# Optimization experiments

Hardware: AMD Instinct MI355X
Metric: run time of the kernel (lower is better)

Reference implementation:

```python
import jax, jax.numpy as jnp
import numpy as np

N_NODES = 50000
NEG_SLOPE = 0.2  # PyG GATConv default leaky-relu slope


def _gat_conv(x, edge_index, W, a_src, a_dst, bias, heads, out_ch, concat, num_nodes):
    # x: [N, F_in]; W: [F_in, heads*out_ch]; a_src/a_dst: [heads, out_ch]; bias: [heads*out_ch] or [out_ch]
    h = (x @ W).reshape(num_nodes, heads, out_ch)            # [N,H,C]
    alpha_src = jnp.einsum('nhc,hc->nh', h, a_src)           # [N,H]
    alpha_dst = jnp.einsum('nhc,hc->nh', h, a_dst)           # [N,H]
    src, dst = edge_index[0], edge_index[1]
    e = jax.nn.leaky_relu(alpha_src[src] + alpha_dst[dst], NEG_SLOPE)  # [E,H]
    # segment softmax over incoming edges per destination (self-loops guarantee non-empty segments)
    m = jax.ops.segment_max(e, dst, num_segments=num_nodes)
    e = jnp.exp(e - m[dst])
    denom = jax.ops.segment_sum(e, dst, num_segments=num_nodes)
    alpha = e / denom[dst]                                    # [E,H]
    msg = h[src] * alpha[:, :, None]                          # [E,H,C]
    out = jax.ops.segment_sum(msg, dst, num_segments=num_nodes)  # [N,H,C]
    if concat:
        out = out.reshape(num_nodes, heads * out_ch)
    else:
        out = out.mean(axis=1)
    return out + bias


def _add_self_loops(edge_index, num_nodes):
    loops = jnp.arange(num_nodes, dtype=edge_index.dtype)
    return jnp.concatenate([edge_index, jnp.stack([loops, loops])], axis=1)


def setup_inputs() -> dict:
    key = jax.random.key(0)
    ks = jax.random.split(key, 16)
    N, F_in, H, C_hid, C_out = N_NODES, 128, 4, 64, 64
    E = 800000
    x = jax.random.normal(ks[0], (N, F_in), dtype=jnp.float32)
    edge_index = jax.random.randint(ks[1], (2, E), 0, N, dtype=jnp.int32)
    s = lambda fan: 1.0 / np.sqrt(fan)
    inp = {
        'x': x, 'edge_index': edge_index,
        'W1': jax.random.normal(ks[2], (F_in, H * C_hid), jnp.float32) * s(F_in),
        'a_src1': jax.random.normal(ks[3], (H, C_hid), jnp.float32) * s(C_hid),
        'a_dst1': jax.random.normal(ks[4], (H, C_hid), jnp.float32) * s(C_hid),
        'b1': jnp.zeros((H * C_hid,), jnp.float32),
        'W2': jax.random.normal(ks[5], (H * C_hid, H * C_hid), jnp.float32) * s(H * C_hid),
        'a_src2': jax.random.normal(ks[6], (H, C_hid), jnp.float32) * s(C_hid),
        'a_dst2': jax.random.normal(ks[7], (H, C_hid), jnp.float32) * s(C_hid),
        'b2': jnp.zeros((H * C_hid,), jnp.float32),
        'W3': jax.random.normal(ks[8], (H * C_hid, C_out), jnp.float32) * s(H * C_hid),
        'a_src3': jax.random.normal(ks[9], (1, C_out), jnp.float32) * s(C_out),
        'a_dst3': jax.random.normal(ks[10], (1, C_out), jnp.float32) * s(C_out),
        'b3': jnp.zeros((C_out,), jnp.float32),
    }
    return inp


def reference(x, edge_index, W1, a_src1, a_dst1, b1, W2, a_src2, a_dst2, b2, W3, a_src3, a_dst3, b3):
    N = x.shape[0]
    ei = _add_self_loops(edge_index, N)
    h = _gat_conv(x, ei, W1, a_src1, a_dst1, b1, heads=4, out_ch=64, concat=True, num_nodes=N)
    h = jax.nn.elu(h)
    h = _gat_conv(h, ei, W2, a_src2, a_dst2, b2, heads=4, out_ch=64, concat=True, num_nodes=N)
    h = jax.nn.elu(h)
    out = _gat_conv(h, ei, W3, a_src3, a_dst3, b3, heads=1, out_ch=64, concat=False, num_nodes=N)
    return out
```

## Files before the change

### kernel.cpp

```cpp
#include <hip/hip_runtime.h>
#include <hip/hip_fp16.h>
#include <cstdint>


typedef _Float16 f16;
typedef _Float16 f16x8 __attribute__((ext_vector_type(8)));
typedef float f32x4 __attribute__((ext_vector_type(4)));

__global__ __launch_bounds__(256) void count_kernel(const int* __restrict__ ei,
                                                    int E, int N,
                                                    int* __restrict__ deg) {
  int g = blockIdx.x * 256 + threadIdx.x;
  if (g >= E + N) return;
  int dst = (g < E) ? ei[E + g] : (g - E);
  atomicAdd(&deg[dst], 1);
}

__global__ __launch_bounds__(256) void deg_block_reduce(const int* __restrict__ deg,
                                                        int* __restrict__ bsum, int N) {
  __shared__ int red[4];
  int b = blockIdx.x;
  int v = 0;
#pragma unroll
  for (int s = 0; s < 4; ++s) {
    int idx = b * 1024 + s * 256 + threadIdx.x;
    if (idx < N) v += deg[idx];
  }
  for (int off = 32; off; off >>= 1) v += __shfl_down(v, off);
  if ((threadIdx.x & 63) == 0) red[threadIdx.x >> 6] = v;
  __syncthreads();
  if (threadIdx.x == 0) bsum[b] = red[0] + red[1] + red[2] + red[3];
}

__global__ __launch_bounds__(1024) void small_scan(const int* __restrict__ bsum,
                                                   int* __restrict__ bpre, int NB) {
  __shared__ int buf[1024];
  int v = (threadIdx.x < NB) ? bsum[threadIdx.x] : 0;
  buf[threadIdx.x] = v;
  __syncthreads();
  for (int off = 1; off < 1024; off <<= 1) {
    int tv = (threadIdx.x >= off) ? buf[threadIdx.x - off] : 0;
    __syncthreads();
    buf[threadIdx.x] += tv;
    __syncthreads();
  }
  if (threadIdx.x < NB) bpre[threadIdx.x] = buf[threadIdx.x] - v;
}

__global__ __launch_bounds__(1024) void scan_final(const int* __restrict__ deg,
                                                   const int* __restrict__ bpre,
                                                   int* __restrict__ row_off,
                                                   int* __restrict__ cursor,
                                                   int N, int total) {
  __shared__ int buf[1024];
  int b = blockIdx.x;
  int i = b * 1024 + threadIdx.x;
  int v = (i < N) ? deg[i] : 0;
  buf[threadIdx.x] = v;
  __syncthreads();
  for (int off = 1; off < 1024; off <<= 1) {
    int tv = (threadIdx.x >= off) ? buf[threadIdx.x - off] : 0;
    __syncthreads();
    buf[threadIdx.x] += tv;
    __syncthreads();
  }
  if (i < N) {
    int ro = bpre[b] + buf[threadIdx.x] - v;
    row_off[i] = ro;
    cursor[i] = ro;
  }
  if (i == 0) row_off[N] = total;
}

__global__ __launch_bounds__(256) void scatter_kernel(const int* __restrict__ ei,
                                                      int E, int N,
                                                      int* __restrict__ cursor,
                                                      int* __restrict__ esrc) {
  int g = blockIdx.x * 256 + threadIdx.x;
  if (g >= E + N) return;
  int src, dst;
  if (g < E) { src = ei[g]; dst = ei[E + g]; }
  else       { src = g - E; dst = src; }
  int pos = atomicAdd(&cursor[dst], 1);
  esrc[pos] = src;
}

__global__ __launch_bounds__(256) void convert_wt(const float* __restrict__ W,
                                                  f16* __restrict__ Wt,
                                                  int K, int Ncol) {
  int t = blockIdx.x * 256 + threadIdx.x;
  if (t >= K * Ncol) return;
  int n = t % Ncol, k = t / Ncol;
  Wt[(size_t)n * K + k] = (f16)W[t];
}

template <int BN, bool ACAST>
__global__ __launch_bounds__(256) void mfma_gemm_alpha(
    const void* __restrict__ Ap_, const f16* __restrict__ Bt,
    f16* __restrict__ Tout,
    const float* __restrict__ avec_src, const float* __restrict__ avec_dst,
    float* __restrict__ asrc, float* __restrict__ adst,
    int M, int K, int Ncol) {
  constexpr int RF = (BN == 128) ? 4 : 2;
  __shared__ f16 As[128][40];
  __shared__ f16 Bs[BN][40];
  int tid = threadIdx.x;
  int wv = tid >> 6, lane = tid & 63;
  int lrow = lane & 15, lkb = lane >> 4;
  int row0 = blockIdx.x * 128, col0 = blockIdx.y * BN;
  int wro = (BN == 128) ? (wv >> 1) * 64 : wv * 32;
  int wco = (BN == 128) ? (wv & 1) * 64 : 0;
  int hg = (col0 + wco) >> 6;

  f32x4 acc[RF][4];
#pragma unroll
  for (int rf = 0; rf < RF; ++rf)
#pragma unroll
    for (int cf = 0; cf < 4; ++cf) acc[rf][cf] = (f32x4){0.f, 0.f, 0.f, 0.f};

  for (int kk = 0; kk < K; kk += 32) {
#pragma unroll
    for (int q = 0; q < 2; ++q) {
      int slot = tid + q * 256;
      int r = slot >> 2, ko = (slot & 3) << 3;
      int gr = min(row0 + r, M - 1);
      if (ACAST) {
        const float* Af = (const float*)Ap_ + (size_t)gr * K + kk + ko;
        float4 v0 = *reinterpret_cast<const float4*>(Af);
        float4 v1 = *reinterpret_cast<const float4*>(Af + 4);
        f16 o[8] = {(f16)v0.x, (f16)v0.y, (f16)v0.z, (f16)v0.w,
                    (f16)v1.x, (f16)v1.y, (f16)v1.z, (f16)v1.w};
        *reinterpret_cast<f16x8*>(&As[r][ko]) = *reinterpret_cast<f16x8*>(o);
      } else {
        *reinterpret_cast<f16x8*>(&As[r][ko]) =
            *reinterpret_cast<const f16x8*>((const f16*)Ap_ + (size_t)gr * K + kk + ko);
      }
    }
#pragma unroll
    for (int q = 0; q < BN / 64; ++q) {
      int slot = tid + q * 256;
      int c = slot >> 2, ko = (slot & 3) << 3;
      *reinterpret_cast<f16x8*>(&Bs[c][ko]) =
          *reinterpret_cast<const f16x8*>(&Bt[(size_t)(col0 + c) * K + kk + ko]);
    }
    __syncthreads();
    f16x8 af[RF], bf[4];
#pragma unroll
    for (int rf = 0; rf < RF; ++rf)
      af[rf] = *reinterpret_cast<f16x8*>(&As[wro + rf * 16 + lrow][lkb * 8]);
#pragma unroll
    for (int cf = 0; cf < 4; ++cf)
      bf[cf] = *reinterpret_cast<f16x8*>(&Bs[wco + cf * 16 + lrow][lkb * 8]);
#pragma unroll
    for (int rf = 0; rf < RF; ++rf)
#pragma unroll
      for (int cf = 0; cf < 4; ++cf)
        acc[rf][cf] = __builtin_amdgcn_mfma_f32_16x16x32_f16(af[rf], bf[cf],
                                                             acc[rf][cf], 0, 0, 0);
    __syncthreads();
  }

  int Hh = Ncol >> 6;
  float avs[4], avd[4];
#pragma unroll
  for (int cf = 0; cf < 4; ++cf) {
    avs[cf] = avec_src[hg * 64 + cf * 16 + lrow];
    avd[cf] = avec_dst[hg * 64 + cf * 16 + lrow];
  }

#pragma unroll
  for (int rf = 0; rf < RF; ++rf) {
#pragma unroll
    for (int r = 0; r < 4; ++r) {
      float ps = 0.f, pd = 0.f;
#pragma unroll
      for (int cf = 0; cf < 4; ++cf) {
        float v = acc[rf][cf][r];
        ps = fmaf(v, avs[cf], ps);
        pd = fmaf(v, avd[cf], pd);
      }
#pragma unroll
      for (int off = 1; off < 16; off <<= 1) {
        ps += __shfl_xor(ps, off);
        pd += __shfl_xor(pd, off);
      }
      int row = row0 + wro + rf * 16 + lkb * 4 + r;
      if (lrow == 0 && row < M) {
        asrc[row * Hh + hg] = ps;
        adst[row * Hh + hg] = pd;
      }
    }
#pragma unroll
    for (int r = 0; r < 4; ++r) {
      int row = row0 + wro + rf * 16 + lkb * 4 + r;
      if (row < M) {
#pragma unroll
        for (int cf = 0; cf < 4; ++cf)
          Tout[(size_t)row * Ncol + col0 + wco + cf * 16 + lrow] =
              (f16)acc[rf][cf][r];
      }
    }
  }
}

template <bool ELU>
__global__ __launch_bounds__(256) void aggregate_h4(
    const f16* __restrict__ T16, const int* __restrict__ row_off,
    const int* __restrict__ esrc, const float* __restrict__ asrc,
    const float* __restrict__ adst, const float* __restrict__ bias,
    f16* __restrict__ outF, int N) {
  int wv = threadIdx.x >> 6, lane = threadIdx.x & 63;
  int dst = blockIdx.x * 4 + wv;
  if (dst >= N) return;
  int head = lane >> 4;
  int we = lane >> 2, wh = lane & 3;
  int ll = lane & 15;
  int r0 = row_off[dst], r1 = row_off[dst + 1];
  float adjh = adst[dst * 4 + wh];
  const char* tbase = reinterpret_cast<const char*>(T16);
  uint loff = (uint)lane * 8;
  float den = 0.f, ax = 0.f, ay = 0.f, az = 0.f, aw = 0.f;
  for (int base = r0; base < r1; base += 16) {
    int cnt = min(16, r1 - base);
    int jb = base + ll;
    int svl = esrc[jb < r1 ? jb : r1 - 1];
    int sw = __shfl(svl, we);
    float e = asrc[sw * 4 + wh] + adjh;
    e = fmaxf(e, 0.2f * e);
    float wl = (we < cnt) ? __expf(e) : 0.f;
#pragma unroll 4
    for (int i = 0; i < cnt; ++i) {
      int sj = __shfl(svl, i);
      float wj = __shfl(wl, (i << 2) + head);
      den += wj;
      uint2 raw = *reinterpret_cast<const uint2*>(tbase + (((uint)sj << 9) + loff));
      __half2 p0 = *reinterpret_cast<__half2*>(&raw.x);
      __half2 p1 = *reinterpret_cast<__half2*>(&raw.y);
      float2 f0 = __half22float2(p0);
      float2 f1 = __half22float2(p1);
      ax = fmaf(wj, f0.x, ax);
      ay = fmaf(wj, f0.y, ay);
      az = fmaf(wj, f1.x, az);
      aw = fmaf(wj, f1.y, aw);
    }
  }
  float rd = 1.f / den;
  float4 bv = *reinterpret_cast<const float4*>(&bias[lane << 2]);
  float vx = ax * rd + bv.x, vy = ay * rd + bv.y;
  float vz = az * rd + bv.z, vw = aw * rd + bv.w;
  if (ELU) {
    vx = vx > 0.f ? vx : expm1f(vx);
    vy = vy > 0.f ? vy : expm1f(vy);
    vz = vz > 0.f ? vz : expm1f(vz);
    vw = vw > 0.f ? vw : expm1f(vw);
  }
  f16 o[4] = {(f16)vx, (f16)vy, (f16)vz, (f16)vw};
  *reinterpret_cast<uint2*>(&outF[(size_t)dst * 256 + (lane << 2)]) =
      *reinterpret_cast<uint2*>(o);
}

__global__ __launch_bounds__(256) void aggregate_h1(
    const f16* __restrict__ T16, const int* __restrict__ row_off,
    const int* __restrict__ esrc, const float* __restrict__ asrc,
    const float* __restrict__ adst, const float* __restrict__ bias,
    float* __restrict__ out, int N) {
  int wv = threadIdx.x >> 6, lane = threadIdx.x & 63;
  int grp = lane >> 4, l = lane & 15;
  int gsel = lane & 48;
  int dst = blockIdx.x * 16 + wv * 4 + grp;
  if (dst >= N) return;
  int r0 = row_off[dst], r1 = row_off[dst + 1];
  float adj = adst[dst];
  const char* tbase = reinterpret_cast<const char*>(T16);
  uint loff = (uint)l * 8;
  float den = 0.f, ax = 0.f, ay = 0.f, az = 0.f, aw = 0.f;
  for (int base = r0; base < r1; base += 16) {
    int cnt = min(16, r1 - base);
    int jb = base + l;
    int svl = esrc[jb < r1 ? jb : r1 - 1];
    float e = asrc[svl] + adj;
    e = fmaxf(e, 0.2f * e);
    float wl = (l < cnt) ? __expf(e) : 0.f;
#pragma unroll 4
    for (int i = 0; i < cnt; ++i) {
      int sj = __shfl(svl, gsel + i);
      float wj = __shfl(wl, gsel + i);
      den += wj;
      uint2 raw = *reinterpret_cast<const uint2*>(tbase + (((uint)sj << 7) + loff));
      __half2 p0 = *reinterpret_cast<__half2*>(&raw.x);
      __half2 p1 = *reinterpret_cast<__half2*>(&raw.y);
      float2 f0 = __half22float2(p0);
      float2 f1 = __half22float2(p1);
      ax = fmaf(wj, f0.x, ax);
      ay = fmaf(wj, f0.y, ay);
      az = fmaf(wj, f1.x, az);
      aw = fmaf(wj, f1.y, aw);
    }
  }
  float rd = 1.f / den;
  float4 v;
  v.x = ax * rd + bias[l * 4 + 0];
  v.y = ay * rd + bias[l * 4 + 1];
  v.z = az * rd + bias[l * 4 + 2];
  v.w = aw * rd + bias[l * 4 + 3];
  *reinterpret_cast<float4*>(&out[(size_t)dst * 64 + l * 4]) = v;
}

extern "C" void kernel_launch(void* const* d_in, const int* in_sizes, int n_in,
                              void* d_out, int out_size, void* d_ws, size_t ws_size,
                              hipStream_t stream) {
  const float* x   = (const float*)d_in[0];
  const int*   ei  = (const int*)d_in[1];
  const float* W1  = (const float*)d_in[2];
  const float* as1 = (const float*)d_in[3];
  const float* ad1 = (const float*)d_in[4];
  const float* b1  = (const float*)d_in[5];
  const float* W2  = (const float*)d_in[6];
  const float* as2 = (const float*)d_in[7];
  const float* ad2 = (const float*)d_in[8];
  const float* b2  = (const float*)d_in[9];
  const float* W3  = (const float*)d_in[10];
  const float* as3 = (const float*)d_in[11];
  const float* ad3 = (const float*)d_in[12];
  const float* b3  = (const float*)d_in[13];
  float* out = (float*)d_out;

  const int Fin = 128, H = 4, C = 64, HC = H * C;
  const int N = in_sizes[0] / Fin;
  const int E = in_sizes[1] / 2;
  const int ET = E + N;
  const int NB = (N + 1023) / 1024;

  f16* T16   = (f16*)d_ws;
  f16* F16   = T16 + (size_t)N * HC;
  f16* T16L3 = F16 + (size_t)N * HC;
  f16* Wt1   = T16L3 + (size_t)N * C;
  f16* Wt2   = Wt1 + HC * Fin;
  f16* Wt3   = Wt2 + HC * HC;
  float* asrc = (float*)(Wt3 + C * HC);
  float* adst = asrc + (size_t)N * H;
  int* deg     = (int*)(adst + (size_t)N * H);
  int* row_off = deg + N;
  int* cursor  = row_off + (N + 1);
  int* bsum    = cursor + N;
  int* bpre    = bsum + NB;
  int* esrc    = bpre + NB;

  hipMemsetAsync(deg, 0, N * sizeof(int), stream);
  count_kernel<<<(ET + 255) / 256, 256, 0, stream>>>(ei, E, N, deg);
  deg_block_reduce<<<NB, 256, 0, stream>>>(deg, bsum, N);
  small_scan<<<1, 1024, 0, stream>>>(bsum, bpre, NB);
  scan_final<<<NB, 1024, 0, stream>>>(deg, bpre, row_off, cursor, N, ET);
  scatter_kernel<<<(ET + 255) / 256, 256, 0, stream>>>(ei, E, N, cursor, esrc);

  convert_wt<<<(Fin * HC + 255) / 256, 256, 0, stream>>>(W1, Wt1, Fin, HC);
  convert_wt<<<(HC * HC + 255) / 256, 256, 0, stream>>>(W2, Wt2, HC, HC);
  convert_wt<<<(HC * C + 255) / 256, 256, 0, stream>>>(W3, Wt3, HC, C);

  int gx = (N + 127) / 128;
  int ab4 = (N + 3) / 4;
  int ab1 = (N + 15) / 16;

  mfma_gemm_alpha<128, true><<<dim3(gx, 2), 256, 0, stream>>>(
      x, Wt1, T16, as1, ad1, asrc, adst, N, Fin, HC);
  aggregate_h4<true><<<ab4, 256, 0, stream>>>(T16, row_off, esrc, asrc, adst, b1, F16, N);

  mfma_gemm_alpha<128, false><<<dim3(gx, 2), 256, 0, stream>>>(
      F16, Wt2, T16, as2, ad2, asrc, adst, N, HC, HC);
  aggregate_h4<true><<<ab4, 256, 0, stream>>>(T16, row_off, esrc, asrc, adst, b2, F16, N);

  mfma_gemm_alpha<64, false><<<dim3(gx, 1), 256, 0, stream>>>(
      F16, Wt3, T16L3, as3, ad3, asrc, adst, N, HC, C);
  aggregate_h1<<<ab1, 256, 0, stream>>>(T16L3, row_off, esrc, asrc, adst, b3, out, N);
}
```

Before: 354.2 us.

## Precompute per-edge attention weights in separate edge-parallel kernels

Moves the leaky-relu and exp attention-logit computation out of the per-destination aggregation kernels into new edge-parallel kernels that write a per-edge weight buffer. Scatter now also records each edge's destination. This takes the dependent gather of asrc by source and the exp off the aggregation's critical path and gives them full edge-level parallelism. The cost is three extra kernel launches, an extra edge-destination array, and an extra pass writing and re-reading about 850K×4 floats per layer.

```diff
diff --git a/kernel.cpp b/kernel.cpp
--- a/kernel.cpp
+++ b/kernel.cpp
@@ -75,7 +75,8 @@
 __global__ __launch_bounds__(256) void scatter_kernel(const int* __restrict__ ei,
                                                       int E, int N,
                                                       int* __restrict__ cursor,
-                                                      int* __restrict__ esrc) {
+                                                      int* __restrict__ esrc,
+                                                      int* __restrict__ edst) {
   int g = blockIdx.x * 256 + threadIdx.x;
   if (g >= E + N) return;
   int src, dst;
@@ -83,6 +84,7 @@
   else       { src = g - E; dst = src; }
   int pos = atomicAdd(&cursor[dst], 1);
   esrc[pos] = src;
+  edst[pos] = dst;
 }
 
 __global__ __launch_bounds__(256) void convert_wt(const float* __restrict__ W,
@@ -203,35 +205,57 @@
   }
 }
 
+__global__ __launch_bounds__(256) void edge_weights_h4(
+    const int* __restrict__ esrc, const int* __restrict__ edst,
+    const float* __restrict__ asrc, const float* __restrict__ adst,
+    float* __restrict__ w, int ET) {
+  int t = blockIdx.x * 256 + threadIdx.x;
+  if (t >= ET * 4) return;
+  int j = t >> 2, h = t & 3;
+  float e = asrc[esrc[j] * 4 + h] + adst[edst[j] * 4 + h];
+  e = fmaxf(e, 0.2f * e);
+  w[t] = __expf(e);
+}
+
+__global__ __launch_bounds__(256) void edge_weights_h1(
+    const int* __restrict__ esrc, const int* __restrict__ edst,
+    const float* __restrict__ asrc, const float* __restrict__ adst,
+    float* __restrict__ w, int ET) {
+  int j = blockIdx.x * 256 + threadIdx.x;
+  if (j >= ET) return;
+  float e = asrc[esrc[j]] + adst[edst[j]];
+  e = fmaxf(e, 0.2f * e);
+  w[j] = __expf(e);
+}
+
 template <bool ELU>
 __global__ __launch_bounds__(256) void aggregate_h4(
     const f16* __restrict__ T16, const int* __restrict__ row_off,
-    const int* __restrict__ esrc, const float* __restrict__ asrc,
-    const float* __restrict__ adst, const float* __restrict__ bias,
-    f16* __restrict__ outF, int N) {
+    const int* __restrict__ esrc, const float* __restrict__ w,
+    const float* __restrict__ bias, f16* __restrict__ outF, int N) {
   int wv = threadIdx.x >> 6, lane = threadIdx.x & 63;
   int dst = blockIdx.x * 4 + wv;
   if (dst >= N) return;
   int head = lane >> 4;
-  int we = lane >> 2, wh = lane & 3;
+  int hsel = lane & 48;
   int ll = lane & 15;
   int r0 = row_off[dst], r1 = row_off[dst + 1];
-  float adjh = adst[dst * 4 + wh];
   const char* tbase = reinterpret_cast<const char*>(T16);
   uint loff = (uint)lane * 8;
   float den = 0.f, ax = 0.f, ay = 0.f, az = 0.f, aw = 0.f;
   for (int base = r0; base < r1; base += 16) {
+    int jb = base + ll;
+    int sv = 0;
+    float wl = 0.f;
+    if (jb < r1) {
+      sv = esrc[jb];
+      wl = w[(jb << 2) + head];
+    }
     int cnt = min(16, r1 - base);
-    int jb = base + ll;
-    int svl = esrc[jb < r1 ? jb : r1 - 1];
-    int sw = __shfl(svl, we);
-    float e = asrc[sw * 4 + wh] + adjh;
-    e = fmaxf(e, 0.2f * e);
-    float wl = (we < cnt) ? __expf(e) : 0.f;
 #pragma unroll 4
     for (int i = 0; i < cnt; ++i) {
-      int sj = __shfl(svl, i);
-      float wj = __shfl(wl, (i << 2) + head);
+      int sj = __shfl(sv, i);
+      float wj = __shfl(wl, hsel + i);
       den += wj;
       uint2 raw = *reinterpret_cast<const uint2*>(tbase + (((uint)sj << 9) + loff));
       __half2 p0 = *reinterpret_cast<__half2*>(&raw.x);
@@ -261,29 +285,29 @@
 
 __global__ __launch_bounds__(256) void aggregate_h1(
     const f16* __restrict__ T16, const int* __restrict__ row_off,
-    const int* __restrict__ esrc, const float* __restrict__ asrc,
-    const float* __restrict__ adst, const float* __restrict__ bias,
-    float* __restrict__ out, int N) {
+    const int* __restrict__ esrc, const float* __restrict__ w,
+    const float* __restrict__ bias, float* __restrict__ out, int N) {
   int wv = threadIdx.x >> 6, lane = threadIdx.x & 63;
   int grp = lane >> 4, l = lane & 15;
   int gsel = lane & 48;
   int dst = blockIdx.x * 16 + wv * 4 + grp;
   if (dst >= N) return;
   int r0 = row_off[dst], r1 = row_off[dst + 1];
-  float adj = adst[dst];
   const char* tbase = reinterpret_cast<const char*>(T16);
   uint loff = (uint)l * 8;
   float den = 0.f, ax = 0.f, ay = 0.f, az = 0.f, aw = 0.f;
   for (int base = r0; base < r1; base += 16) {
+    int jb = base + l;
+    int sv = 0;
+    float wl = 0.f;
+    if (jb < r1) {
+      sv = esrc[jb];
+      wl = w[jb];
+    }
     int cnt = min(16, r1 - base);
-    int jb = base + l;
-    int svl = esrc[jb < r1 ? jb : r1 - 1];
-    float e = asrc[svl] + adj;
-    e = fmaxf(e, 0.2f * e);
-    float wl = (l < cnt) ? __expf(e) : 0.f;
 #pragma unroll 4
     for (int i = 0; i < cnt; ++i) {
-      int sj = __shfl(svl, gsel + i);
+      int sj = __shfl(sv, gsel + i);
       float wj = __shfl(wl, gsel + i);
       den += wj;
       uint2 raw = *reinterpret_cast<const uint2*>(tbase + (((uint)sj << 7) + loff));
@@ -339,37 +363,43 @@
   f16* Wt3   = Wt2 + HC * HC;
   float* asrc = (float*)(Wt3 + C * HC);
   float* adst = asrc + (size_t)N * H;
-  int* deg     = (int*)(adst + (size_t)N * H);
+  float* wbuf = adst + (size_t)N * H;
+  int* deg     = (int*)(wbuf + (size_t)ET * 4);
   int* row_off = deg + N;
   int* cursor  = row_off + (N + 1);
   int* bsum    = cursor + N;
   int* bpre    = bsum + NB;
   int* esrc    = bpre + NB;
+  int* edst    = esrc + ET;
 
   hipMemsetAsync(deg, 0, N * sizeof(int), stream);
   count_kernel<<<(ET + 255) / 256, 256, 0, stream>>>(ei, E, N, deg);
   deg_block_reduce<<<NB, 256, 0, stream>>>(deg, bsum, N);
   small_scan<<<1, 1024, 0, stream>>>(bsum, bpre, NB);
   scan_final<<<NB, 1024, 0, stream>>>(deg, bpre, row_off, cursor, N, ET);
-  scatter_kernel<<<(ET + 255) / 256, 256, 0, stream>>>(ei, E, N, cursor, esrc);
+  scatter_kernel<<<(ET + 255) / 256, 256, 0, stream>>>(ei, E, N, cursor, esrc, edst);
 
   convert_wt<<<(Fin * HC + 255) / 256, 256, 0, stream>>>(W1, Wt1, Fin, HC);
   convert_wt<<<(HC * HC + 255) / 256, 256, 0, stream>>>(W2, Wt2, HC, HC);
   convert_wt<<<(HC * C + 255) / 256, 256, 0, stream>>>(W3, Wt3, HC, C);
 
   int gx = (N + 127) / 128;
+  int eb4 = (ET * 4 + 255) / 256, eb1 = (ET + 255) / 256;
   int ab4 = (N + 3) / 4;
   int ab1 = (N + 15) / 16;
 
   mfma_gemm_alpha<128, true><<<dim3(gx, 2), 256, 0, stream>>>(
       x, Wt1, T16, as1, ad1, asrc, adst, N, Fin, HC);
-  aggregate_h4<true><<<ab4, 256, 0, stream>>>(T16, row_off, esrc, asrc, adst, b1, F16, N);
+  edge_weights_h4<<<eb4, 256, 0, stream>>>(esrc, edst, asrc, adst, wbuf, ET);
+  aggregate_h4<true><<<ab4, 256, 0, stream>>>(T16, row_off, esrc, wbuf, b1, F16, N);
 
   mfma_gemm_alpha<128, false><<<dim3(gx, 2), 256, 0, stream>>>(
       F16, Wt2, T16, as2, ad2, asrc, adst, N, HC, HC);
-  aggregate_h4<true><<<ab4, 256, 0, stream>>>(T16, row_off, esrc, asrc, adst, b2, F16, N);
+  edge_weights_h4<<<eb4, 256, 0, stream>>>(esrc, edst, asrc, adst, wbuf, ET);
+  aggregate_h4<true><<<ab4, 256, 0, stream>>>(T16, row_off, esrc, wbuf, b2, F16, N);
 
   mfma_gemm_alpha<64, false><<<dim3(gx, 1), 256, 0, stream>>>(
       F16, Wt3, T16L3, as3, ad3, asrc, adst, N, HC, C);
-  aggregate_h1<<<ab1, 256, 0, stream>>>(T16L3, row_off, esrc, asrc, adst, b3, out, N);
-}
+  edge_weights_h1<<<eb1, 256, 0, stream>>>(esrc, edst, asrc, adst, wbuf, ET);
+  aggregate_h1<<<ab1, 256, 0, stream>>>(T16L3, row_off, esrc, wbuf, b3, out, N);
+}
```

Result: slower. 368.3 us (+4.0%).
